# Kernel tuning notes

Measured on AMD Instinct MI355X. Metric: run time of the kernel, lower is better.

## Reference

```python
import jax, jax.numpy as jnp
import numpy as np

B, D, H, N, M, K = 128, 256, 4, 256, 256, 10  # M=256 is hardcoded in the original repeat(1,1,1,256)
DIM = D // H  # per-head dim = 64


def setup_inputs() -> dict:
    key = jax.random.key(0)
    ks = jax.random.split(key, 10)
    s = 0.05  # weight scale
    return {
        "x": jax.random.normal(ks[0], (B, D, N), jnp.float32),
        "source": jax.random.normal(ks[1], (B, D, M), jnp.float32),
        "Wq": jax.random.normal(ks[2], (D, D), jnp.float32) * s,
        "bq": jax.random.normal(ks[3], (D,), jnp.float32) * s,
        "Wk": jax.random.normal(ks[4], (D, D), jnp.float32) * s,
        "bk": jax.random.normal(ks[5], (D,), jnp.float32) * s,
        "Wv": jax.random.normal(ks[6], (D, D), jnp.float32) * s,
        "bv": jax.random.normal(ks[7], (D,), jnp.float32) * s,
        "Wm": jax.random.normal(ks[8], (D, D), jnp.float32) * s,
        "bm": jax.random.normal(ks[9], (D,), jnp.float32) * s,
        "k": K,
    }


def _pointwise(W, b, x):
    # nn.Conv1d(d, d, kernel_size=1): per-point linear over channel dim
    return jnp.einsum('ef,bfn->ben', W, x) + b[None, :, None]


def reference(x, source, Wq, bq, Wk, bk, Wv, bv, Wm, bm, k):
    b, d, n = x.shape
    # torch .view(b, dim, heads, -1) splits channels as (dim, heads)
    q = _pointwise(Wq, bq, x).reshape(b, DIM, H, n)
    kk = _pointwise(Wk, bk, source).reshape(b, DIM, H, -1)
    v = _pointwise(Wv, bv, source).reshape(b, DIM, H, -1)

    scores = jnp.einsum('bdhn,bdhm->bhnm', q, kk) / jnp.sqrt(jnp.asarray(DIM, x.dtype))
    # per-row top-k threshold: keep only scores >= k-th largest, softmax over kept
    thresh = jax.lax.top_k(scores, k)[0][..., k - 1:k]  # [b,h,n,1]
    mask = scores >= thresh
    neg = jnp.finfo(scores.dtype).min
    prob = jax.nn.softmax(jnp.where(mask, scores, neg), axis=-1)
    prob = jnp.where(mask, prob, jnp.zeros((), scores.dtype))

    out = jnp.einsum('bhnm,bdhm->bdhn', prob, v).reshape(b, d, n)
    return _pointwise(Wm, bm, out)
```

## Files before the change

### kernel.cpp

```cpp
#include <hip/hip_runtime.h>
#include <hip/hip_bf16.h>

#define BB   128
#define DDIM 256
#define HH   4
#define NNN  256
#define MMM  256

typedef __hip_bfloat16 bf16;
typedef short  short8   __attribute__((ext_vector_type(8)));
typedef unsigned short ushort8_t __attribute__((ext_vector_type(8)));
typedef float  f32x4    __attribute__((ext_vector_type(4)));
typedef float  f32x2    __attribute__((ext_vector_type(2)));

__device__ __forceinline__ unsigned short f2bf(float x) {
    unsigned u = __builtin_bit_cast(unsigned, x);
    u += 0x7FFFu + ((u >> 16) & 1u);
    return (unsigned short)(u >> 16);
}
__device__ __forceinline__ float bf2f(unsigned short b) {
    unsigned u = ((unsigned)b) << 16;
    return __builtin_bit_cast(float, u);
}

__device__ __forceinline__ void xpose4(float v[4], const int p) {
    float ta = __shfl_xor((p & 1) ? v[0] : v[1], 1, 64);
    float tb = __shfl_xor((p & 1) ? v[2] : v[3], 1, 64);
    float u0 = (p & 1) ? ta : v[0];
    float u1 = (p & 1) ? v[1] : ta;
    float u2 = (p & 1) ? tb : v[2];
    float u3 = (p & 1) ? v[3] : tb;
    float tc = __shfl_xor((p & 2) ? u0 : u2, 2, 64);
    float td = __shfl_xor((p & 2) ? u1 : u3, 2, 64);
    v[0] = (p & 2) ? tc : u0;
    v[1] = (p & 2) ? td : u1;
    v[2] = (p & 2) ? u2 : tc;
    v[3] = (p & 2) ? u3 : td;
}

__device__ __forceinline__ void split3_store8k(char* dst, const float v[4]) {
    unsigned short h[4], m[4], l[4];
    #pragma unroll
    for (int i = 0; i < 4; ++i) {
        h[i] = f2bf(v[i]);
        float r1 = v[i] - bf2f(h[i]);
        m[i] = f2bf(r1);
        float r2 = r1 - bf2f(m[i]);
        l[i] = f2bf(r2);
    }
    uint2 hp, mp, lp;
    hp.x = (unsigned)h[0] | ((unsigned)h[1] << 16);
    hp.y = (unsigned)h[2] | ((unsigned)h[3] << 16);
    mp.x = (unsigned)m[0] | ((unsigned)m[1] << 16);
    mp.y = (unsigned)m[2] | ((unsigned)m[3] << 16);
    lp.x = (unsigned)l[0] | ((unsigned)l[1] << 16);
    lp.y = (unsigned)l[2] | ((unsigned)l[3] << 16);
    *(uint2*)dst = hp;
    *(uint2*)(dst + 8192) = mp;
    *(uint2*)(dst + 16384) = lp;
}

__device__ __forceinline__ void split2_store(char* dst, const float v[4]) {
    unsigned short h[4], m[4];
    #pragma unroll
    for (int i = 0; i < 4; ++i) {
        h[i] = f2bf(v[i]);
        float r1 = v[i] - bf2f(h[i]);
        m[i] = f2bf(r1);
    }
    uint2 hp, mp;
    hp.x = (unsigned)h[0] | ((unsigned)h[1] << 16);
    hp.y = (unsigned)h[2] | ((unsigned)h[3] << 16);
    mp.x = (unsigned)m[0] | ((unsigned)m[1] << 16);
    mp.y = (unsigned)m[2] | ((unsigned)m[3] << 16);
    *(uint2*)dst = hp;
    *(uint2*)(dst + 16384) = mp;
}

__device__ __forceinline__ void ldx4(const float* p, float v[4]) {
    const float4 f = *(const float4*)p;
    v[0] = f.x; v[1] = f.y; v[2] = f.z; v[3] = f.w;
}
__device__ __forceinline__ void ldx4(const bf16* p, float v[4]) {
    uint2 u = *(const uint2*)p;
    v[0] = bf2f((unsigned short)(u.x & 0xFFFF));
    v[1] = bf2f((unsigned short)(u.x >> 16));
    v[2] = bf2f((unsigned short)(u.y & 0xFFFF));
    v[3] = bf2f((unsigned short)(u.y >> 16));
}

__device__ __forceinline__ float max16v(const float* w) {
    float a = fmaxf(fmaxf(w[0], w[1]),  fmaxf(w[2], w[3]));
    float b = fmaxf(fmaxf(w[4], w[5]),  fmaxf(w[6], w[7]));
    float c = fmaxf(fmaxf(w[8], w[9]),  fmaxf(w[10], w[11]));
    float d = fmaxf(fmaxf(w[12], w[13]), fmaxf(w[14], w[15]));
    return fmaxf(fmaxf(a, b), fmaxf(c, d));
}
__device__ __forceinline__ float gmax16(float v) {
    v = fmaxf(v, __shfl_xor(v, 1, 64));
    v = fmaxf(v, __shfl_xor(v, 2, 64));
    v = fmaxf(v, __shfl_xor(v, 4, 64));
    v = fmaxf(v, __shfl_xor(v, 8, 64));
    return v;
}
__device__ __forceinline__ float gsum16(float v) {
    v += __shfl_xor(v, 1, 64);
    v += __shfl_xor(v, 2, 64);
    v += __shfl_xor(v, 4, 64);
    v += __shfl_xor(v, 8, 64);
    return v;
}

template <int MODE>
__global__ __launch_bounds__(256)
void projqk_kernel(const float* __restrict__ X, const float* __restrict__ W,
                   const float* __restrict__ bias, float* __restrict__ Yt,
                   unsigned short* __restrict__ Ph, unsigned short* __restrict__ Pm,
                   unsigned short* __restrict__ Pl) {
    __shared__ float Wt[32][268];
    __shared__ float Xt[32][36];

    const int t  = threadIdx.x;
    const int tx = t & 7;
    const int ty = t >> 3;
    const int n0 = blockIdx.x * 32;
    const int b  = blockIdx.y;
    const size_t plane = (size_t)b * DDIM * NNN;

    f32x2 acc2[8][2];
    #pragma unroll
    for (int i = 0; i < 8; ++i) {
        acc2[i][0] = f32x2{0.f, 0.f};
        acc2[i][1] = f32x2{0.f, 0.f};
    }

    for (int f0 = 0; f0 < DDIM; f0 += 32) {
        #pragma unroll
        for (int i = 0; i < 8; ++i) {
            int idx = t + i * 256;
            int fq = idx & 7, el = idx >> 3;
            const float4 w4 = *(const float4*)&W[(size_t)el * DDIM + f0 + fq * 4];
            Wt[fq * 4 + 0][el] = w4.x;
            Wt[fq * 4 + 1][el] = w4.y;
            Wt[fq * 4 + 2][el] = w4.z;
            Wt[fq * 4 + 3][el] = w4.w;
        }
        #pragma unroll
        for (int i = 0; i < 4; ++i) {
            int idx = t + i * 256;
            int fl = idx >> 5, nl = idx & 31;
            Xt[fl][nl] = X[plane + (size_t)(f0 + fl) * NNN + n0 + nl];
        }
        __syncthreads();

        #pragma unroll
        for (int ff = 0; ff < 32; ++ff) {
            const float4 av0 = *(const float4*)&Wt[ff][ty * 8];
            const float4 av1 = *(const float4*)&Wt[ff][ty * 8 + 4];
            const float4 bv  = *(const float4*)&Xt[ff][tx * 4];
            const float a[8] = {av0.x, av0.y, av0.z, av0.w, av1.x, av1.y, av1.z, av1.w};
            const f32x2 c0 = {bv.x, bv.y};
            const f32x2 c1 = {bv.z, bv.w};
            #pragma unroll
            for (int i2 = 0; i2 < 8; ++i2) {
                const f32x2 aa = {a[i2], a[i2]};
                acc2[i2][0] = __builtin_elementwise_fma(aa, c0, acc2[i2][0]);
                acc2[i2][1] = __builtin_elementwise_fma(aa, c1, acc2[i2][1]);
            }
        }
        __syncthreads();
    }

    float* stage = &Wt[0][0];
    #pragma unroll
    for (int i2 = 0; i2 < 8; ++i2) {
        const int e = ty * 8 + i2;
        const float bs = bias[e];
        const int col = (e & 3) * 64 + (e >> 2);
        stage[(tx * 4 + 0) * 260 + col] = acc2[i2][0].x + bs;
        stage[(tx * 4 + 1) * 260 + col] = acc2[i2][0].y + bs;
        stage[(tx * 4 + 2) * 260 + col] = acc2[i2][1].x + bs;
        stage[(tx * 4 + 3) * 260 + col] = acc2[i2][1].y + bs;
    }
    __syncthreads();

    #pragma unroll
    for (int it = 0; it < 8; ++it) {
        int gid = t + it * 256;
        int n   = gid >> 6;
        int sub = gid & 63;
        const float4 v4 = *(const float4*)&stage[n * 260 + sub * 4];
        const int hh = sub >> 4;
        const int dd0 = (sub & 15) * 4;
        const size_t off = ((size_t)(b * 4 + hh) * NNN + n0 + n) * 64 + dd0;
        if constexpr (MODE == 0) {
            *(float4*)&Yt[off] = v4;
        } else {
            const float v[4] = {v4.x, v4.y, v4.z, v4.w};
            unsigned short h[4], m[4], l[4];
            #pragma unroll
            for (int i = 0; i < 4; ++i) {
                h[i] = f2bf(v[i]);
                float r1 = v[i] - bf2f(h[i]);
                m[i] = f2bf(r1);
                float r2 = r1 - bf2f(m[i]);
                l[i] = f2bf(r2);
            }
            uint2 hp, mp, lp;
            hp.x = (unsigned)h[0] | ((unsigned)h[1] << 16);
            hp.y = (unsigned)h[2] | ((unsigned)h[3] << 16);
            mp.x = (unsigned)m[0] | ((unsigned)m[1] << 16);
            mp.y = (unsigned)m[2] | ((unsigned)m[3] << 16);
            lp.x = (unsigned)l[0] | ((unsigned)l[1] << 16);
            lp.y = (unsigned)l[2] | ((unsigned)l[3] << 16);
            *(uint2*)&Ph[off] = hp;
            *(uint2*)&Pm[off] = mp;
            *(uint2*)&Pl[off] = lp;
        }
    }
}

__global__ __launch_bounds__(256, 4)
void attn4_kernel(const float* __restrict__ qt,
                  const unsigned short* __restrict__ khp,
                  const unsigned short* __restrict__ kmp,
                  const unsigned short* __restrict__ klp,
                  const bf16* __restrict__ vb, bf16* __restrict__ ob,
                  const int* __restrict__ kptr) {
    extern __shared__ __align__(16) char smem[];

    const int t    = threadIdx.x;
    const int lane = t & 63;
    const int w    = t >> 6;
    const int g    = lane >> 4;
    const int c16  = lane & 15;

    const int i    = blockIdx.x;
    const int work = (i & 7) * 256 + (i >> 3);
    const int bx = work & 3;
    const int h  = (work >> 2) & 3;
    const int b  = work >> 4;
    const int n0 = bx * 64;
    const int bh = b * 4 + h;

    const size_t planeV = (size_t)b * DDIM * MMM;

    int kk = kptr[0];
    kk = kk < 1 ? 1 : (kk > MMM ? MMM : kk);

    #pragma unroll
    for (int it = 0; it < 4; ++it) {
        int gid = t + it * 256;
        int dq = gid & 15;
        int n  = gid >> 4;
        const float4 q4 = *(const float4*)&qt[((size_t)bh * NNN + n0 + n) * 64 + dq * 4];
        float v[4] = {q4.x * 0.125f, q4.y * 0.125f, q4.z * 0.125f, q4.w * 0.125f};
        int base = n * 128 + ((dq * 8) ^ ((n & 7) << 4));
        split3_store8k(smem + base, v);
    }
    __syncthreads();

    short8 qh[2], qm[2], ql[2];
    #pragma unroll
    for (int ks = 0; ks < 2; ++ks) {
        int nl = w * 16 + c16;
        int off = nl * 128 + ((ks * 64 + g * 16) ^ ((nl & 7) << 4));
        qh[ks] = *(const short8*)(smem + off);
        qm[ks] = *(const short8*)(smem + 8192 + off);
        ql[ks] = *(const short8*)(smem + 16384 + off);
    }
    __syncthreads();

    f32x4 acc[16];
    #pragma unroll
    for (int m = 0; m < 16; ++m) acc[m] = f32x4{0.f, 0.f, 0.f, 0.f};

    #pragma unroll
    for (int tt = 0; tt < 4; ++tt) {
        if (tt) __syncthreads();
        #pragma unroll
        for (int it = 0; it < 6; ++it) {
            int gid = t + it * 256;
            int pl  = gid >> 9;
            int rem = gid & 511;
            int ml  = rem >> 3;
            int dq  = rem & 7;
            int dqs = dq ^ (ml & 7);
            const unsigned short* kp = (pl == 0) ? khp : (pl == 1 ? kmp : klp);
            const unsigned short* src = kp + ((size_t)bh * MMM + tt * 64 + ml) * 64 + dqs * 8;
            __builtin_amdgcn_global_load_lds(
                (const __attribute__((address_space(1))) void*)src,
                (__attribute__((address_space(3))) void*)(smem + gid * 16),
                16, 0, 0);
        }
        __syncthreads();

        #pragma unroll
        for (int mf = 0; mf < 4; ++mf) {
            #pragma unroll
            for (int ks = 0; ks < 2; ++ks) {
                int ml = mf * 16 + c16;
                int off = ml * 128 + ((ks * 64 + g * 16) ^ ((ml & 7) << 4));
                short8 bh_ = *(const short8*)(smem + off);
                short8 bm_ = *(const short8*)(smem + 8192 + off);
                short8 bl_ = *(const short8*)(smem + 16384 + off);
                f32x4 a = acc[tt * 4 + mf];
                a = __builtin_amdgcn_mfma_f32_16x16x32_bf16(qh[ks], bh_, a, 0, 0, 0);
                a = __builtin_amdgcn_mfma_f32_16x16x32_bf16(qh[ks], bm_, a, 0, 0, 0);
                a = __builtin_amdgcn_mfma_f32_16x16x32_bf16(qm[ks], bh_, a, 0, 0, 0);
                a = __builtin_amdgcn_mfma_f32_16x16x32_bf16(qm[ks], bm_, a, 0, 0, 0);
                a = __builtin_amdgcn_mfma_f32_16x16x32_bf16(qh[ks], bl_, a, 0, 0, 0);
                a = __builtin_amdgcn_mfma_f32_16x16x32_bf16(ql[ks], bh_, a, 0, 0, 0);
                acc[tt * 4 + mf] = a;
            }
        }
    }
    __syncthreads();

    float thr[4], rmx[4];
    #pragma unroll
    for (int r = 0; r < 4; ++r) {
        float w16[16];
        #pragma unroll
        for (int mf = 0; mf < 16; ++mf) w16[mf] = acc[mf][r];
        float lm = max16v(w16);
        float gm = gmax16(lm);
        rmx[r] = gm;
        for (int it = 1; it < kk; ++it) {
            unsigned long long bal = __ballot(lm == gm);
            unsigned gmask = (unsigned)((bal >> (g * 16)) & 0xFFFFull);
            int leader = __builtin_ctz(gmask);
            bool skip = (c16 != leader);
            #pragma unroll
            for (int mf = 0; mf < 16; ++mf) {
                bool hit = (!skip) && (w16[mf] == gm);
                w16[mf] = hit ? -INFINITY : w16[mf];
                skip = skip || hit;
            }
            lm = max16v(w16);
            gm = gmax16(lm);
        }
        thr[r] = gm;
    }

    #pragma unroll
    for (int mf = 0; mf < 16; ++mf) {
        #pragma unroll
        for (int r = 0; r < 4; ++r) {
            float a = acc[mf][r];
            acc[mf][r] = (a >= thr[r]) ? __expf(a - rmx[r]) : 0.f;
        }
    }
    float inv_[4];
    #pragma unroll
    for (int r = 0; r < 4; ++r) {
        float s = ((acc[0][r] + acc[1][r]) + (acc[2][r] + acc[3][r]))
                + ((acc[4][r] + acc[5][r]) + (acc[6][r] + acc[7][r]))
                + ((acc[8][r] + acc[9][r]) + (acc[10][r] + acc[11][r]))
                + ((acc[12][r] + acc[13][r]) + (acc[14][r] + acc[15][r]));
        s = gsum16(s);
        inv_[r] = 1.0f / s;
    }
    #pragma unroll
    for (int mf = 0; mf < 16; ++mf) {
        #pragma unroll
        for (int r = 0; r < 4; ++r) {
            int row = w * 16 + g * 4 + r;
            int m2  = (mf * 16 + c16) * 2;
            int off = row * 512 + (m2 ^ ((row & 7) << 4));
            *(unsigned short*)(smem + off) = f2bf(acc[mf][r] * inv_[r]);
        }
    }
    __syncthreads();

    f32x4 o[4];
    #pragma unroll
    for (int df = 0; df < 4; ++df) o[df] = f32x4{0.f, 0.f, 0.f, 0.f};

    #pragma unroll
    for (int half = 0; half < 2; ++half) {
        short8 pa[4];
        #pragma unroll
        for (int ks = 0; ks < 4; ++ks) {
            int row = w * 16 + c16;
            int off = row * 512 + ((half * 256 + ks * 64 + g * 16) ^ ((row & 7) << 4));
            pa[ks] = *(const short8*)(smem + off);
        }
        #pragma unroll
        for (int df = 0; df < 4; ++df) {
            int d = df * 16 + c16;
            const bf16* vrow = vb + planeV + (size_t)(d * HH + h) * MMM + half * 128;
            f32x4 o_ = o[df];
            #pragma unroll
            for (int ks = 0; ks < 4; ++ks) {
                short8 vv = *(const short8*)(vrow + ks * 32 + g * 8);
                o_ = __builtin_amdgcn_mfma_f32_16x16x32_bf16(pa[ks], vv, o_, 0, 0, 0);
            }
            o[df] = o_;
        }
    }
    __syncthreads();

    #pragma unroll
    for (int df = 0; df < 4; ++df)
        #pragma unroll
        for (int r = 0; r < 4; ++r) {
            int d  = df * 16 + c16;
            int nl = w * 16 + g * 4 + r;
            int off = d * 128 + ((nl * 2) ^ ((d & 7) << 4));
            *(unsigned short*)(smem + off) = f2bf(o[df][r]);
        }
    __syncthreads();
    #pragma unroll
    for (int it = 0; it < 2; ++it) {
        int idx = t + it * 256;
        int d = idx >> 3, ch = idx & 7;
        int off = d * 128 + ((ch * 16) ^ ((d & 7) << 4));
        ushort8_t val = *(const ushort8_t*)(smem + off);
        *(ushort8_t*)&ob[planeV + (size_t)(d * HH + h) * NNN + n0 + ch * 8] = val;
    }
}

template <typename TIN, typename TOUT>
__global__ __launch_bounds__(512, 2)
void projm_kernel(const TIN* __restrict__ X, const float* __restrict__ W,
                  const float* __restrict__ bias, TOUT* __restrict__ Y) {
    extern __shared__ __align__(16) char smem[];

    const int t    = threadIdx.x;
    const int lane = t & 63;
    const int w    = t >> 6;
    const int c16  = lane & 15;
    const int g    = (lane >> 4) & 3;
    const int p    = lane & 3;
    const int G    = lane >> 2;

    const int n0 = blockIdx.x * 128;
    const int e0 = blockIdx.y * 128;
    const int b  = blockIdx.z;
    const size_t plane = (size_t)b * DDIM * NNN;

    f32x4 acc[8];
    #pragma unroll
    for (int nf = 0; nf < 8; ++nf) acc[nf] = f32x4{0.f, 0.f, 0.f, 0.f};

    #pragma unroll
    for (int ft = 0; ft < 4; ++ft) {
        const int f0 = ft * 64;
        if (ft) __syncthreads();
        #pragma unroll
        for (int it = 0; it < 4; ++it) {
            int chunk = w + 8 * it;
            int fch = chunk & 15, nh = chunk >> 4;
            float v[4];
            ldx4(&X[plane + (size_t)(f0 + fch * 4 + p) * NNN + n0 + nh * 64 + G * 4], v);
            xpose4(v, p);
            int nl = nh * 64 + G * 4 + p;
            int base = nl * 128 + ((fch * 8) ^ ((nl & 7) << 4));
            split2_store(smem + base, v);
        }
        #pragma unroll
        for (int it = 0; it < 4; ++it) {
            int idx = t + 512 * it;
            int el = idx >> 4, fq = idx & 15;
            float v[4];
            const float4 f4 = *(const float4*)&W[(size_t)(e0 + el) * DDIM + f0 + fq * 4];
            v[0] = f4.x; v[1] = f4.y; v[2] = f4.z; v[3] = f4.w;
            int base = 32768 + el * 128 + ((fq * 8) ^ ((el & 7) << 4));
            split2_store(smem + base, v);
        }
        __syncthreads();

        const int ew = w * 16;
        short8 a0[2], a1[2];
        #pragma unroll
        for (int ks = 0; ks < 2; ++ks) {
            int off = 32768 + (ew + c16) * 128
                    + ((ks * 64 + g * 16) ^ ((c16 & 7) << 4));
            a0[ks] = *(const short8*)(smem + off);
            a1[ks] = *(const short8*)(smem + off + 16384);
        }
        #pragma unroll
        for (int nf = 0; nf < 8; ++nf) {
            #pragma unroll
            for (int ks = 0; ks < 2; ++ks) {
                int off = (nf * 16 + c16) * 128
                        + ((ks * 64 + g * 16) ^ ((c16 & 7) << 4));
                short8 b0 = *(const short8*)(smem + off);
                short8 b1 = *(const short8*)(smem + off + 16384);
                f32x4 a = acc[nf];
                a = __builtin_amdgcn_mfma_f32_16x16x32_bf16(a0[ks], b0, a, 0, 0, 0);
                a = __builtin_amdgcn_mfma_f32_16x16x32_bf16(a0[ks], b1, a, 0, 0, 0);
                a = __builtin_amdgcn_mfma_f32_16x16x32_bf16(a1[ks], b0, a, 0, 0, 0);
                acc[nf] = a;
            }
        }
    }

    const int ew = w * 16;
    float bs[4];
    #pragma unroll
    for (int r = 0; r < 4; ++r) bs[r] = bias[e0 + ew + g * 4 + r];
    #pragma unroll
    for (int nf = 0; nf < 8; ++nf) {
        #pragma unroll
        for (int r = 0; r < 4; ++r) {
            size_t off = plane + (size_t)(e0 + ew + g * 4 + r) * NNN + n0 + nf * 16 + c16;
            float val = acc[nf][r] + bs[r];
            if constexpr (sizeof(TOUT) == 4) Y[off] = val;
            else                             *(unsigned short*)&Y[off] = f2bf(val);
        }
    }
}

extern "C" void kernel_launch(void* const* d_in, const int* in_sizes, int n_in,
                              void* d_out, int out_size, void* d_ws, size_t ws_size,
                              hipStream_t stream) {
    const float* x   = (const float*)d_in[0];
    const float* src = (const float*)d_in[1];
    const float* Wq  = (const float*)d_in[2];
    const float* bq  = (const float*)d_in[3];
    const float* Wk  = (const float*)d_in[4];
    const float* bk  = (const float*)d_in[5];
    const float* Wv  = (const float*)d_in[6];
    const float* bv  = (const float*)d_in[7];
    const float* Wm  = (const float*)d_in[8];
    const float* bm  = (const float*)d_in[9];
    const int*   kp  = (const int*)d_in[10];
    float* out = (float*)d_out;

    char* ws = (char*)d_ws;
    const size_t QT_BYTES = 33554432;
    const size_t PL_BYTES = 16777216;

    float*          qt = (float*)(ws);
    unsigned short* kh = (unsigned short*)(ws + QT_BYTES);
    unsigned short* km = (unsigned short*)(ws + QT_BYTES + PL_BYTES);
    unsigned short* kl = (unsigned short*)(ws + QT_BYTES + 2 * PL_BYTES);
    bf16*           vb = (bf16*)(ws + QT_BYTES + 3 * PL_BYTES);
    bf16*           ob = (bf16*)(ws + QT_BYTES + 4 * PL_BYTES);

    hipFuncSetAttribute((const void*)(projm_kernel<float, bf16>),
                        hipFuncAttributeMaxDynamicSharedMemorySize, 65536);
    hipFuncSetAttribute((const void*)(projm_kernel<bf16, float>),
                        hipFuncAttributeMaxDynamicSharedMemorySize, 65536);
    hipFuncSetAttribute((const void*)attn4_kernel,
                        hipFuncAttributeMaxDynamicSharedMemorySize, 32768);

    dim3 qk_grid(NNN / 32, BB);
    dim3 mgrid(2, 2, BB);

    hipLaunchKernelGGL((projqk_kernel<0>), qk_grid, dim3(256), 0, stream,
                       x,   Wq, bq, qt, nullptr, nullptr, nullptr);
    hipLaunchKernelGGL((projqk_kernel<1>), qk_grid, dim3(256), 0, stream,
                       src, Wk, bk, nullptr, kh, km, kl);
    hipLaunchKernelGGL((projm_kernel<float, bf16>), mgrid, dim3(512), 65536, stream,
                       src, Wv, bv, vb);
    hipLaunchKernelGGL(attn4_kernel, dim3(2048), dim3(256), 32768, stream,
                       qt, kh, km, kl, vb, ob, kp);
    hipLaunchKernelGGL((projm_kernel<bf16, float>), mgrid, dim3(512), 65536, stream,
                       ob, Wm, bm, out);
}
```

Before: 289.9 us.

## Store Q projection in natural layout and transpose in attention; skip bf16 residual for bf16 input

The Q projection moves to a new tiled FP32 GEMM kernel that writes the natural [b, d, n] layout. The attention kernel now reads Q per channel-row and transposes it in registers with xpose4 before the 3-way bf16 split, so the heavy transposing staging epilogue of the old projection is gone. The output projection, whose input is already bf16, now stores only the high part of X and drops one MFMA per step, which also shrinks its shared memory. The max16v reduction tree is reordered as well. The risk is less coalesced Q loads inside attention, and the new Q GEMM may be slower than the old one.

Measured after the change: 264.8 us (median of 2 runs). 8.7% less time.

```diff
diff --git a/kernel.cpp b/kernel.cpp
--- a/kernel.cpp
+++ b/kernel.cpp
@@ -77,6 +77,13 @@
     *(uint2*)(dst + 16384) = mp;
 }
 
+__device__ __forceinline__ void split1_store(char* dst, const float v[4]) {
+    uint2 hp;
+    hp.x = (unsigned)f2bf(v[0]) | ((unsigned)f2bf(v[1]) << 16);
+    hp.y = (unsigned)f2bf(v[2]) | ((unsigned)f2bf(v[3]) << 16);
+    *(uint2*)dst = hp;
+}
+
 __device__ __forceinline__ void ldx4(const float* p, float v[4]) {
     const float4 f = *(const float4*)p;
     v[0] = f.x; v[1] = f.y; v[2] = f.z; v[3] = f.w;
@@ -90,11 +97,14 @@
 }
 
 __device__ __forceinline__ float max16v(const float* w) {
-    float a = fmaxf(fmaxf(w[0], w[1]),  fmaxf(w[2], w[3]));
-    float b = fmaxf(fmaxf(w[4], w[5]),  fmaxf(w[6], w[7]));
-    float c = fmaxf(fmaxf(w[8], w[9]),  fmaxf(w[10], w[11]));
-    float d = fmaxf(fmaxf(w[12], w[13]), fmaxf(w[14], w[15]));
-    return fmaxf(fmaxf(a, b), fmaxf(c, d));
+    float a = fmaxf(fmaxf(w[0],  w[1]),  w[2]);
+    float b = fmaxf(fmaxf(w[3],  w[4]),  w[5]);
+    float c = fmaxf(fmaxf(w[6],  w[7]),  w[8]);
+    float d = fmaxf(fmaxf(w[9],  w[10]), w[11]);
+    float e = fmaxf(fmaxf(w[12], w[13]), w[14]);
+    float ab = fmaxf(fmaxf(a, b), c);
+    float de = fmaxf(fmaxf(d, e), w[15]);
+    return fmaxf(ab, de);
 }
 __device__ __forceinline__ float gmax16(float v) {
     v = fmaxf(v, __shfl_xor(v, 1, 64));
@@ -111,12 +121,71 @@
     return v;
 }
 
-template <int MODE>
 __global__ __launch_bounds__(256)
-void projqk_kernel(const float* __restrict__ X, const float* __restrict__ W,
-                   const float* __restrict__ bias, float* __restrict__ Yt,
-                   unsigned short* __restrict__ Ph, unsigned short* __restrict__ Pm,
-                   unsigned short* __restrict__ Pl) {
+void proj_kernel(const float* __restrict__ X, const float* __restrict__ W,
+                 const float* __restrict__ bias, float* __restrict__ Y) {
+    __shared__ float Wt[32][68];
+    __shared__ float Xt[32][132];
+
+    const int t  = threadIdx.x;
+    const int tx = t & 31;
+    const int ty = t >> 5;
+    const int n0 = blockIdx.x * 128;
+    const int e0 = blockIdx.y * 64;
+    const int b  = blockIdx.z;
+    const size_t plane = (size_t)b * DDIM * NNN;
+
+    float acc[8][4] = {};
+
+    for (int f0 = 0; f0 < DDIM; f0 += 32) {
+        #pragma unroll
+        for (int i = 0; i < 8; ++i) {
+            int idx = t + i * 256;
+            int fl = idx & 31, el = idx >> 5;
+            Wt[fl][el] = W[(size_t)(e0 + el) * DDIM + f0 + fl];
+        }
+        #pragma unroll
+        for (int i = 0; i < 4; ++i) {
+            int idx = t + i * 256;
+            int fl = idx >> 5, nl4 = idx & 31;
+            *(float4*)&Xt[fl][nl4 * 4] =
+                *(const float4*)&X[plane + (size_t)(f0 + fl) * NNN + n0 + nl4 * 4];
+        }
+        __syncthreads();
+
+        #pragma unroll
+        for (int ff = 0; ff < 32; ++ff) {
+            const float4 av0 = *(const float4*)&Wt[ff][ty * 8];
+            const float4 av1 = *(const float4*)&Wt[ff][ty * 8 + 4];
+            const float4 bv  = *(const float4*)&Xt[ff][tx * 4];
+            const float a[8] = {av0.x, av0.y, av0.z, av0.w, av1.x, av1.y, av1.z, av1.w};
+            const float c[4] = {bv.x, bv.y, bv.z, bv.w};
+            #pragma unroll
+            for (int i2 = 0; i2 < 8; ++i2)
+                #pragma unroll
+                for (int j = 0; j < 4; ++j)
+                    acc[i2][j] = fmaf(a[i2], c[j], acc[i2][j]);
+        }
+        __syncthreads();
+    }
+
+    #pragma unroll
+    for (int i2 = 0; i2 < 8; ++i2) {
+        const int e = e0 + ty * 8 + i2;
+        const float bs = bias[e];
+        const size_t off = plane + (size_t)e * NNN + n0 + tx * 4;
+        float4 o;
+        o.x = acc[i2][0] + bs; o.y = acc[i2][1] + bs;
+        o.z = acc[i2][2] + bs; o.w = acc[i2][3] + bs;
+        *(float4*)&Y[off] = o;
+    }
+}
+
+__global__ __launch_bounds__(256)
+void projk_kernel(const float* __restrict__ X, const float* __restrict__ W,
+                  const float* __restrict__ bias,
+                  unsigned short* __restrict__ Ph, unsigned short* __restrict__ Pm,
+                  unsigned short* __restrict__ Pl) {
     __shared__ float Wt[32][268];
     __shared__ float Xt[32][36];
 
@@ -193,35 +262,31 @@
         const int hh = sub >> 4;
         const int dd0 = (sub & 15) * 4;
         const size_t off = ((size_t)(b * 4 + hh) * NNN + n0 + n) * 64 + dd0;
-        if constexpr (MODE == 0) {
-            *(float4*)&Yt[off] = v4;
-        } else {
-            const float v[4] = {v4.x, v4.y, v4.z, v4.w};
-            unsigned short h[4], m[4], l[4];
-            #pragma unroll
-            for (int i = 0; i < 4; ++i) {
-                h[i] = f2bf(v[i]);
-                float r1 = v[i] - bf2f(h[i]);
-                m[i] = f2bf(r1);
-                float r2 = r1 - bf2f(m[i]);
-                l[i] = f2bf(r2);
-            }
-            uint2 hp, mp, lp;
-            hp.x = (unsigned)h[0] | ((unsigned)h[1] << 16);
-            hp.y = (unsigned)h[2] | ((unsigned)h[3] << 16);
-            mp.x = (unsigned)m[0] | ((unsigned)m[1] << 16);
-            mp.y = (unsigned)m[2] | ((unsigned)m[3] << 16);
-            lp.x = (unsigned)l[0] | ((unsigned)l[1] << 16);
-            lp.y = (unsigned)l[2] | ((unsigned)l[3] << 16);
-            *(uint2*)&Ph[off] = hp;
-            *(uint2*)&Pm[off] = mp;
-            *(uint2*)&Pl[off] = lp;
-        }
+        const float v[4] = {v4.x, v4.y, v4.z, v4.w};
+        unsigned short h[4], m[4], l[4];
+        #pragma unroll
+        for (int i = 0; i < 4; ++i) {
+            h[i] = f2bf(v[i]);
+            float r1 = v[i] - bf2f(h[i]);
+            m[i] = f2bf(r1);
+            float r2 = r1 - bf2f(m[i]);
+            l[i] = f2bf(r2);
+        }
+        uint2 hp, mp, lp;
+        hp.x = (unsigned)h[0] | ((unsigned)h[1] << 16);
+        hp.y = (unsigned)h[2] | ((unsigned)h[3] << 16);
+        mp.x = (unsigned)m[0] | ((unsigned)m[1] << 16);
+        mp.y = (unsigned)m[2] | ((unsigned)m[3] << 16);
+        lp.x = (unsigned)l[0] | ((unsigned)l[1] << 16);
+        lp.y = (unsigned)l[2] | ((unsigned)l[3] << 16);
+        *(uint2*)&Ph[off] = hp;
+        *(uint2*)&Pm[off] = mp;
+        *(uint2*)&Pl[off] = lp;
     }
 }
 
 __global__ __launch_bounds__(256, 4)
-void attn4_kernel(const float* __restrict__ qt,
+void attn4_kernel(const float* __restrict__ qf,
                   const unsigned short* __restrict__ khp,
                   const unsigned short* __restrict__ kmp,
                   const unsigned short* __restrict__ klp,
@@ -243,20 +308,27 @@
     const int n0 = bx * 64;
     const int bh = b * 4 + h;
 
+    const size_t planeF = (size_t)b * DDIM * NNN;
     const size_t planeV = (size_t)b * DDIM * MMM;
 
     int kk = kptr[0];
     kk = kk < 1 ? 1 : (kk > MMM ? MMM : kk);
 
-    #pragma unroll
-    for (int it = 0; it < 4; ++it) {
-        int gid = t + it * 256;
-        int dq = gid & 15;
-        int n  = gid >> 4;
-        const float4 q4 = *(const float4*)&qt[((size_t)bh * NNN + n0 + n) * 64 + dq * 4];
-        float v[4] = {q4.x * 0.125f, q4.y * 0.125f, q4.z * 0.125f, q4.w * 0.125f};
-        int base = n * 128 + ((dq * 8) ^ ((n & 7) << 4));
-        split3_store8k(smem + base, v);
+    {
+        const int p = lane & 3, G = lane >> 2;
+        #pragma unroll
+        for (int it = 0; it < 4; ++it) {
+            int dch = w + 4 * it;
+            int drow = dch * 4 + p;
+            float v[4];
+            const float4 f4 = *(const float4*)&qf[planeF + (size_t)(drow * HH + h) * NNN + n0 + G * 4];
+            v[0] = f4.x * 0.125f; v[1] = f4.y * 0.125f;
+            v[2] = f4.z * 0.125f; v[3] = f4.w * 0.125f;
+            xpose4(v, p);
+            int nl = G * 4 + p;
+            int base = nl * 128 + ((dch * 8) ^ ((nl & 7) << 4));
+            split3_store8k(smem + base, v);
+        }
     }
     __syncthreads();
 
@@ -426,6 +498,8 @@
 void projm_kernel(const TIN* __restrict__ X, const float* __restrict__ W,
                   const float* __restrict__ bias, TOUT* __restrict__ Y) {
     extern __shared__ __align__(16) char smem[];
+    constexpr bool XBF = (sizeof(TIN) == 2);
+    constexpr int WOFF = XBF ? 16384 : 32768;
 
     const int t    = threadIdx.x;
     const int lane = t & 63;
@@ -457,7 +531,8 @@
             xpose4(v, p);
             int nl = nh * 64 + G * 4 + p;
             int base = nl * 128 + ((fch * 8) ^ ((nl & 7) << 4));
-            split2_store(smem + base, v);
+            if constexpr (XBF) split1_store(smem + base, v);
+            else               split2_store(smem + base, v);
         }
         #pragma unroll
         for (int it = 0; it < 4; ++it) {
@@ -466,7 +541,7 @@
             float v[4];
             const float4 f4 = *(const float4*)&W[(size_t)(e0 + el) * DDIM + f0 + fq * 4];
             v[0] = f4.x; v[1] = f4.y; v[2] = f4.z; v[3] = f4.w;
-            int base = 32768 + el * 128 + ((fq * 8) ^ ((el & 7) << 4));
+            int base = WOFF + el * 128 + ((fq * 8) ^ ((el & 7) << 4));
             split2_store(smem + base, v);
         }
         __syncthreads();
@@ -475,7 +550,7 @@
         short8 a0[2], a1[2];
         #pragma unroll
         for (int ks = 0; ks < 2; ++ks) {
-            int off = 32768 + (ew + c16) * 128
+            int off = WOFF + (ew + c16) * 128
                     + ((ks * 64 + g * 16) ^ ((c16 & 7) << 4));
             a0[ks] = *(const short8*)(smem + off);
             a1[ks] = *(const short8*)(smem + off + 16384);
@@ -487,10 +562,12 @@
                 int off = (nf * 16 + c16) * 128
                         + ((ks * 64 + g * 16) ^ ((c16 & 7) << 4));
                 short8 b0 = *(const short8*)(smem + off);
-                short8 b1 = *(const short8*)(smem + off + 16384);
                 f32x4 a = acc[nf];
                 a = __builtin_amdgcn_mfma_f32_16x16x32_bf16(a0[ks], b0, a, 0, 0, 0);
-                a = __builtin_amdgcn_mfma_f32_16x16x32_bf16(a0[ks], b1, a, 0, 0, 0);
+                if constexpr (!XBF) {
+                    short8 b1 = *(const short8*)(smem + off + 16384);
+                    a = __builtin_amdgcn_mfma_f32_16x16x32_bf16(a0[ks], b1, a, 0, 0, 0);
+                }
                 a = __builtin_amdgcn_mfma_f32_16x16x32_bf16(a1[ks], b0, a, 0, 0, 0);
                 acc[nf] = a;
             }
@@ -530,34 +607,35 @@
     float* out = (float*)d_out;
 
     char* ws = (char*)d_ws;
-    const size_t QT_BYTES = 33554432;
+    const size_t QF_BYTES = 33554432;
     const size_t PL_BYTES = 16777216;
 
-    float*          qt = (float*)(ws);
-    unsigned short* kh = (unsigned short*)(ws + QT_BYTES);
-    unsigned short* km = (unsigned short*)(ws + QT_BYTES + PL_BYTES);
-    unsigned short* kl = (unsigned short*)(ws + QT_BYTES + 2 * PL_BYTES);
-    bf16*           vb = (bf16*)(ws + QT_BYTES + 3 * PL_BYTES);
-    bf16*           ob = (bf16*)(ws + QT_BYTES + 4 * PL_BYTES);
+    float*          qf = (float*)(ws);
+    unsigned short* kh = (unsigned short*)(ws + QF_BYTES);
+    unsigned short* km = (unsigned short*)(ws + QF_BYTES + PL_BYTES);
+    unsigned short* kl = (unsigned short*)(ws + QF_BYTES + 2 * PL_BYTES);
+    bf16*           vb = (bf16*)(ws + QF_BYTES + 3 * PL_BYTES);
+    bf16*           ob = (bf16*)(ws + QF_BYTES + 4 * PL_BYTES);
 
     hipFuncSetAttribute((const void*)(projm_kernel<float, bf16>),
                         hipFuncAttributeMaxDynamicSharedMemorySize, 65536);
     hipFuncSetAttribute((const void*)(projm_kernel<bf16, float>),
-                        hipFuncAttributeMaxDynamicSharedMemorySize, 65536);
+                        hipFuncAttributeMaxDynamicSharedMemorySize, 49152);
     hipFuncSetAttribute((const void*)attn4_kernel,
                         hipFuncAttributeMaxDynamicSharedMemorySize, 32768);
 
-    dim3 qk_grid(NNN / 32, BB);
+    dim3 qgrid(NNN / 128, DDIM / 64, BB);
+    dim3 kgrid(NNN / 32, BB);
     dim3 mgrid(2, 2, BB);
 
-    hipLaunchKernelGGL((projqk_kernel<0>), qk_grid, dim3(256), 0, stream,
-                       x,   Wq, bq, qt, nullptr, nullptr, nullptr);
-    hipLaunchKernelGGL((projqk_kernel<1>), qk_grid, dim3(256), 0, stream,
-                       src, Wk, bk, nullptr, kh, km, kl);
+    hipLaunchKernelGGL(proj_kernel, qgrid, dim3(256), 0, stream,
+                       x,   Wq, bq, qf);
+    hipLaunchKernelGGL(projk_kernel, kgrid, dim3(256), 0, stream,
+                       src, Wk, bk, kh, km, kl);
     hipLaunchKernelGGL((projm_kernel<float, bf16>), mgrid, dim3(512), 65536, stream,
                        src, Wv, bv, vb);
     hipLaunchKernelGGL(attn4_kernel, dim3(2048), dim3(256), 32768, stream,
-                       qt, kh, km, kl, vb, ob, kp);
-    hipLaunchKernelGGL((projm_kernel<bf16, float>), mgrid, dim3(512), 65536, stream,
+                       qf, kh, km, kl, vb, ob, kp);
+    hipLaunchKernelGGL((projm_kernel<bf16, float>), mgrid, dim3(512), 49152, stream,
                        ob, Wm, bm, out);
 }
```
